# Kernel tuning notes

Measured on AMD Instinct MI355X. Metric: run time of the kernel, lower is better.

The kernel has to match this reference:

```python
import jax, jax.numpy as jnp
import numpy as np

EPS_NORM = 1e-12   # F.normalize default eps
EPS_ABS = 1e-08


def _l2_normalize(x, axis):
    n = jnp.sqrt(jnp.sum(x * x, axis=axis, keepdims=True))
    return x / jnp.maximum(n, EPS_NORM)


def setup_inputs() -> dict:
    key = jax.random.key(0)
    k1, k2 = jax.random.split(key)
    B, D, H, W = 32, 256, 32, 32
    S = 2048
    features = jax.random.normal(k1, (B, D, H, W), dtype=jnp.float32)
    memory = jax.random.truncated_normal(k2, -2.0, 2.0, (S, D), dtype=jnp.float32) * 0.02
    return {"features": features, "memory": memory}


def reference(features, memory):
    shrink_threshold = 0.0025
    shrink_gamma = 2.0
    temperature = 0.05
    B, D, H, W = features.shape
    S = memory.shape[0]

    # (B,D,H,W) -> (B*H*W, D)
    query = jnp.transpose(features, (0, 2, 3, 1)).reshape(B * H * W, D)

    # addressing: cosine similarity / temperature -> softmax over slots
    q = _l2_normalize(query, axis=1)
    m = _l2_normalize(memory, axis=1)
    sim = (q @ m.T) / temperature                      # [N, S]
    weights = jax.nn.softmax(sim, axis=1)

    # retrieval + soft shrinkage
    retrieved = weights @ memory                       # [N, D]
    a = jnp.abs(retrieved)
    lam = jnp.clip(shrink_gamma * shrink_threshold / (a + EPS_ABS), 0.0, 1.0)
    retrieved = jnp.sign(retrieved) * jax.nn.relu(a * (1.0 - lam))

    # entropy of addressing weights
    entropy = -jnp.mean(jnp.sum(weights * jnp.log(weights + EPS_ABS), axis=1))

    retrieved = jnp.transpose(retrieved.reshape(B, H, W, D), (0, 3, 1, 2))
    weights_image = weights.reshape(B, H * W, S).mean(axis=1)
    return retrieved, entropy, weights_image
```

## Files before the change

kernel.cpp:

```cpp
#include <hip/hip_runtime.h>
#include <cstdint>
#include <cstddef>

#define D_DIM 256
#define S_SLOTS 2048
#define HW_PIX 1024
#define OUT_ENT_IDX 8388608
#define OUT_WIMG_IDX 8388609

using short8 = __attribute__((ext_vector_type(8))) short;
using f32x4  = __attribute__((ext_vector_type(4))) float;

__device__ __forceinline__ unsigned short f2bf(float x) {
    union { float f; unsigned u; } v; v.f = x;
    unsigned r = v.u + 0x7FFF + ((v.u >> 16) & 1);
    return (unsigned short)(r >> 16);
}
__device__ __forceinline__ unsigned pack2(float lo, float hi) {
    return (unsigned)f2bf(lo) | ((unsigned)f2bf(hi) << 16);
}
__device__ __forceinline__ void gload16(const void* g, void* l) {
    __builtin_amdgcn_global_load_lds(
        (const __attribute__((address_space(1))) unsigned int*)g,
        (__attribute__((address_space(3))) unsigned int*)l, 16, 0, 0);
}

__global__ __launch_bounds__(64) void k_prep(const float* __restrict__ mem,
                                             unsigned short* __restrict__ mhatg,
                                             unsigned short* __restrict__ mblkg) {
    const int s = blockIdx.x;
    const int l = threadIdx.x;
    const float4 v = reinterpret_cast<const float4*>(mem + (size_t)s * D_DIM)[l];
    float ss = v.x*v.x + v.y*v.y + v.z*v.z + v.w*v.w;
#pragma unroll
    for (int o = 32; o > 0; o >>= 1) ss += __shfl_xor(ss, o);
    const float sc = 20.0f / fmaxf(sqrtf(ss), 1e-12f);
    {
        ushort4 o;
        o.x = f2bf(v.x*sc); o.y = f2bf(v.y*sc); o.z = f2bf(v.z*sc); o.w = f2bf(v.w*sc);
        const int chunk = (l >> 1) ^ (s & 7);
        char* dst = (char*)mhatg + (size_t)s * 512 + (chunk << 4) + 8 * (l & 1);
        *reinterpret_cast<ushort4*>(dst) = o;
    }
    {
        const int tile = s >> 6, sloc = s & 63;
        char* base = (char*)mblkg + (size_t)tile * 32768;
        const float vv[4] = {v.x, v.y, v.z, v.w};
#pragma unroll
        for (int i = 0; i < 4; ++i) {
            const int d = 4*l + i;
            const int byteoff = d * 128 + ((sloc * 2) ^ ((d & 7) << 4));
            *reinterpret_cast<unsigned short*>(base + byteoff) = f2bf(vv[i]);
        }
    }
}

__device__ __forceinline__ void qkt(const char* mh, const short8 (&qfrag)[2][8],
                                    int srow, int g, int l15, f32x4 (&acc)[2][2]) {
#pragma unroll
    for (int kk = 0; kk < 8; ++kk) {
        const int c0 = ((4*kk + g) ^ (l15 & 7)) << 4;
        const short8 a0 = *reinterpret_cast<const short8*>(mh + srow*512 + c0);
        const short8 a1 = *reinterpret_cast<const short8*>(mh + (srow+16)*512 + c0);
        acc[0][0] = __builtin_amdgcn_mfma_f32_16x16x32_bf16(a0, qfrag[0][kk], acc[0][0], 0,0,0);
        acc[0][1] = __builtin_amdgcn_mfma_f32_16x16x32_bf16(a0, qfrag[1][kk], acc[0][1], 0,0,0);
        acc[1][0] = __builtin_amdgcn_mfma_f32_16x16x32_bf16(a1, qfrag[0][kk], acc[1][0], 0,0,0);
        acc[1][1] = __builtin_amdgcn_mfma_f32_16x16x32_bf16(a1, qfrag[1][kk], acc[1][1], 0,0,0);
    }
}

__global__ __launch_bounds__(512, 2) void k_main(
    const float* __restrict__ feat, const char* __restrict__ mhat_g,
    const char* __restrict__ mblk_g, float* __restrict__ out)
{
    extern __shared__ char dyn[];
    __shared__ float sm_norm[512];
    __shared__ float qs_lds[128];
    __shared__ float zb[2][4][2][16];
    __shared__ float ub[2][4][2][16];
    __shared__ float rZbuf[128];
    __shared__ float entb[4];

    const int tid  = threadIdx.x;
    const int lane = tid & 63;
    const int w    = tid >> 6;
    const int wq   = w & 3;
    const int ws   = w >> 2;
    const int l15  = lane & 15;
    const int g    = (lane >> 4) & 3;
    const int blk  = blockIdx.x;
    const int b    = blk >> 3;
    const int p0   = (blk & 7) * 128;
    const float* fbase = feat + (size_t)b * (D_DIM * HW_PIX);
    float* wimg_g = out + OUT_WIMG_IDX;

    {
        const int dp = tid >> 7, pp = tid & 127;
        const float* fp = fbase + (size_t)(dp*64)*HW_PIX + p0 + pp;
        float ss = 0.f;
#pragma unroll 8
        for (int d = 0; d < 64; ++d) { const float v = fp[(size_t)d*HW_PIX]; ss += v*v; }
        sm_norm[dp*128 + pp] = ss;
    }
    __syncthreads();
    if (tid < 128) {
        const float n2 = sm_norm[tid] + sm_norm[128+tid] + sm_norm[256+tid] + sm_norm[384+tid];
        qs_lds[tid] = 1.0f / fmaxf(sqrtf(n2), 1e-12f);
    }
    __syncthreads();

    short8 qfrag[2][8];
#pragma unroll
    for (int tq = 0; tq < 2; ++tq) {
        const int q = 32*wq + 16*tq + l15;
        const float qs = qs_lds[q];
        const float* fq = fbase + p0 + q;
#pragma unroll
        for (int kk = 0; kk < 8; ++kk) {
            union { short8 s; unsigned u[4]; } fr;
#pragma unroll
            for (int jp = 0; jp < 4; ++jp) {
                const int d = 32*kk + 8*g + 2*jp;
                fr.u[jp] = pack2(fq[(size_t)d*HW_PIX] * qs, fq[(size_t)(d+1)*HW_PIX] * qs);
            }
            qfrag[tq][kk] = fr.s;
        }
    }

    const int srow = 32*ws + l15;

    float Zp[2] = {0.f, 0.f}, Up[2] = {0.f, 0.f};
    for (int st = 0; st < 32; ++st) {
        const char* gsrc = mhat_g + (size_t)st * 32768;
#pragma unroll
        for (int i = 0; i < 4; ++i)
            gload16(gsrc + tid*16 + i*8192, dyn + tid*16 + i*8192);
        __syncthreads();
        f32x4 acc[2][2] = {};
        qkt(dyn, qfrag, srow, g, l15, acc);
#pragma unroll
        for (int ts = 0; ts < 2; ++ts)
#pragma unroll
            for (int tq = 0; tq < 2; ++tq)
#pragma unroll
                for (int r = 0; r < 4; ++r) {
                    const float sim = acc[ts][tq][r];
                    const float e = __expf(sim);
                    Zp[tq] += e; Up[tq] += e * sim;
                }
        __syncthreads();
    }
#pragma unroll
    for (int tq = 0; tq < 2; ++tq) {
        Zp[tq] += __shfl_xor(Zp[tq], 16); Zp[tq] += __shfl_xor(Zp[tq], 32);
        Up[tq] += __shfl_xor(Up[tq], 16); Up[tq] += __shfl_xor(Up[tq], 32);
    }
    if (lane < 16) {
#pragma unroll
        for (int tq = 0; tq < 2; ++tq) {
            zb[ws][wq][tq][lane] = Zp[tq];
            ub[ws][wq][tq][lane] = Up[tq];
        }
    }
    __syncthreads();
    float rZ[2], rZw[2];
    {
        float Zf[2], Uf[2];
#pragma unroll
        for (int tq = 0; tq < 2; ++tq) {
            Zf[tq] = Zp[tq] + zb[1-ws][wq][tq][l15];
            Uf[tq] = Up[tq] + ub[1-ws][wq][tq][l15];
            rZ[tq] = 1.0f / Zf[tq];
            rZw[tq] = rZ[tq] * (1.0f/1024.0f);
        }
        if (ws == 0 && lane < 16) {
            rZbuf[32*wq + l15]      = rZ[0];
            rZbuf[32*wq + 16 + l15] = rZ[1];
            float ent = 0.f;
#pragma unroll
            for (int tq = 0; tq < 2; ++tq) ent += __logf(Zf[tq]) - Uf[tq] * rZ[tq];
            ent += __shfl_xor(ent, 1); ent += __shfl_xor(ent, 2);
            ent += __shfl_xor(ent, 4); ent += __shfl_xor(ent, 8);
            if (lane == 0) entb[wq] = ent;
        }
    }
    __syncthreads();
    if (tid == 0)
        atomicAdd(out + OUT_ENT_IDX, (entb[0]+entb[1]+entb[2]+entb[3]) * (1.0f/32768.0f));

    f32x4 acc_o[2][16] = {};
    for (int st = 0; st < 32; ++st) {
        const char* gsrcA = mhat_g + (size_t)st * 32768;
        const char* gsrcB = mblk_g + (size_t)st * 32768;
#pragma unroll
        for (int i = 0; i < 4; ++i) {
            gload16(gsrcA + tid*16 + i*8192, dyn + tid*16 + i*8192);
            gload16(gsrcB + tid*16 + i*8192, dyn + 33792 + tid*16 + i*8192);
        }
        __syncthreads();
        f32x4 acc[2][2] = {};
        qkt(dyn, qfrag, srow, g, l15, acc);
        float ev[2][2][4];
#pragma unroll
        for (int ts = 0; ts < 2; ++ts)
#pragma unroll
            for (int tq = 0; tq < 2; ++tq)
#pragma unroll
                for (int r = 0; r < 4; ++r)
                    ev[ts][tq][r] = __expf(acc[ts][tq][r]);
        __syncthreads();
#pragma unroll
        for (int ts = 0; ts < 2; ++ts)
#pragma unroll
            for (int tq = 0; tq < 2; ++tq) {
                const int q = 32*wq + 16*tq + l15;
#pragma unroll
                for (int r = 0; r < 4; ++r) {
                    const int s = 32*ws + 16*ts + 4*g + r;
                    *reinterpret_cast<float*>(dyn + s*528 + q*4) = ev[ts][tq][r] * rZw[tq];
                }
            }
        __syncthreads();
        {
            const int s_r = tid >> 3, qc = tid & 7;
            const char* pr = dyn + s_r*528 + qc*64;
            float ps = 0.f;
#pragma unroll
            for (int i = 0; i < 4; ++i) {
                const f32x4 v = *reinterpret_cast<const f32x4*>(pr + i*16);
                ps += v[0] + v[1] + v[2] + v[3];
            }
            ps += __shfl_xor(ps, 1); ps += __shfl_xor(ps, 2); ps += __shfl_xor(ps, 4);
            if (qc == 0) atomicAdd(wimg_g + (size_t)b*2048 + st*64 + s_r, ps);
        }
        short8 pfrag[2];
#pragma unroll
        for (int tq = 0; tq < 2; ++tq) {
            const unsigned u00 = pack2(ev[0][tq][0], ev[0][tq][1]);
            const unsigned u01 = pack2(ev[0][tq][2], ev[0][tq][3]);
            const unsigned u10 = pack2(ev[1][tq][0], ev[1][tq][1]);
            const unsigned u11 = pack2(ev[1][tq][2], ev[1][tq][3]);
            const int sA = l15 + 32*(g & 1);
            const int sB = sA + 16;
            const unsigned a00 = __shfl((int)u00, sA), a10 = __shfl((int)u10, sA);
            const unsigned a01 = __shfl((int)u01, sA), a11 = __shfl((int)u11, sA);
            const unsigned b00 = __shfl((int)u00, sB), b10 = __shfl((int)u10, sB);
            const unsigned b01 = __shfl((int)u01, sB), b11 = __shfl((int)u11, sB);
            const bool hi = (lane & 32) != 0;
            union { short8 s; unsigned u[4]; } fr;
            fr.u[0] = hi ? a10 : a00;
            fr.u[1] = hi ? a11 : a01;
            fr.u[2] = hi ? b10 : b00;
            fr.u[3] = hi ? b11 : b01;
            pfrag[tq] = fr.s;
        }
#pragma unroll
        for (int Dt = 0; Dt < 16; ++Dt) {
            const int d = 16*Dt + l15;
            const int byteoff = 33792 + d*128 + (((4*ws + g) ^ (l15 & 7)) << 4);
            const short8 bf = *reinterpret_cast<const short8*>(dyn + byteoff);
            acc_o[0][Dt] = __builtin_amdgcn_mfma_f32_16x16x32_bf16(pfrag[0], bf, acc_o[0][Dt], 0,0,0);
            acc_o[1][Dt] = __builtin_amdgcn_mfma_f32_16x16x32_bf16(pfrag[1], bf, acc_o[1][Dt], 0,0,0);
        }
        __syncthreads();
    }

    float rZq[2][4];
#pragma unroll
    for (int tq = 0; tq < 2; ++tq)
#pragma unroll
        for (int r = 0; r < 4; ++r)
            rZq[tq][r] = rZbuf[32*wq + 16*tq + 4*g + r];

#pragma unroll
    for (int Dt = 0; Dt < 16; ++Dt) {
        if (ws == 1) {
#pragma unroll
            for (int tq = 0; tq < 2; ++tq)
                *reinterpret_cast<f32x4*>(dyn + ((wq*2 + tq)*64 + lane)*16) = acc_o[tq][Dt];
        }
        __syncthreads();
        if (ws == 0) {
#pragma unroll
            for (int tq = 0; tq < 2; ++tq) {
                const f32x4 other = *reinterpret_cast<const f32x4*>(dyn + ((wq*2 + tq)*64 + lane)*16);
#pragma unroll
                for (int r = 0; r < 4; ++r) {
                    const float o = (acc_o[tq][Dt][r] + other[r]) * rZq[tq][r];
                    const float a = fabsf(o);
                    const float lam = fminf(0.005f / (a + 1e-8f), 1.0f);
                    const float val = copysignf(a * (1.0f - lam), o);
                    const int q = 32*wq + 16*tq + 4*g + r;
                    *reinterpret_cast<float*>(dyn + 8192 + q*84 + l15*4) = val;
                }
            }
        }
        __syncthreads();
#pragma unroll
        for (int i = 0; i < 4; ++i) {
            const int flat = i*512 + tid;
            const int dd = flat >> 7, q = flat & 127;
            const float val = *reinterpret_cast<const float*>(dyn + 8192 + q*84 + dd*4);
            out[((size_t)b*256 + Dt*16 + dd)*HW_PIX + p0 + q] = val;
        }
        __syncthreads();
    }
}

extern "C" void kernel_launch(void* const* d_in, const int* in_sizes, int n_in,
                              void* d_out, int out_size, void* d_ws, size_t ws_size,
                              hipStream_t stream) {
    const float* feat = (const float*)d_in[0];
    const float* mem  = (const float*)d_in[1];
    float* out = (float*)d_out;

    unsigned short* mhat_g = (unsigned short*)d_ws;
    unsigned short* mblk_g = (unsigned short*)((char*)d_ws + (1 << 20));

    hipMemsetAsync((char*)d_out + (size_t)OUT_ENT_IDX * 4, 0,
                   (size_t)(1 + 32 * S_SLOTS) * 4, stream);

    k_prep<<<S_SLOTS, 64, 0, stream>>>(mem, mhat_g, mblk_g);

    const int lds_bytes = 66560;
    hipFuncSetAttribute((const void*)k_main,
                        hipFuncAttributeMaxDynamicSharedMemorySize, lds_bytes);
    k_main<<<256, 512, lds_bytes, stream>>>(feat, (const char*)mhat_g,
                                            (const char*)mblk_g, out);
}
```

Before: 240.8 us.

## Double-buffer memory tiles in LDS, accumulate weights_image in LDS, coalesce prep

Both passes over the memory slots now use double-buffered LDS tiles, with the next tile's async global-to-LDS load issued before computing on the current one. This removes one barrier per iteration and hides load latency. The weights_image column sums now come from wave shuffles into a per-block LDS array, flushed once to global with atomics, replacing the LDS transpose, two extra barriers and per-tile global atomics. The prep kernel stages eight rows in LDS so it can write full 16-byte swizzled chunks with 256 blocks. The cost is a much larger dynamic LDS footprint, which limits residency to one block per CU.

After: 241.9 us. No clear change (+0.5%).

```diff
diff --git a/kernel.cpp b/kernel.cpp
--- a/kernel.cpp
+++ b/kernel.cpp
@@ -8,6 +8,11 @@
 #define OUT_ENT_IDX 8388608
 #define OUT_WIMG_IDX 8388609
 
+#define BUFA_OFF(b) ((b) * 32768)
+#define BUFB_OFF(b) (65536 + (b) * 32768)
+#define WIMG_OFF    131072
+#define DYN_BYTES   139264
+
 using short8 = __attribute__((ext_vector_type(8))) short;
 using f32x4  = __attribute__((ext_vector_type(4))) float;
 
@@ -28,30 +33,49 @@
 __global__ __launch_bounds__(64) void k_prep(const float* __restrict__ mem,
                                              unsigned short* __restrict__ mhatg,
                                              unsigned short* __restrict__ mblkg) {
-    const int s = blockIdx.x;
-    const int l = threadIdx.x;
-    const float4 v = reinterpret_cast<const float4*>(mem + (size_t)s * D_DIM)[l];
-    float ss = v.x*v.x + v.y*v.y + v.z*v.z + v.w*v.w;
-#pragma unroll
-    for (int o = 32; o > 0; o >>= 1) ss += __shfl_xor(ss, o);
-    const float sc = 20.0f / fmaxf(sqrtf(ss), 1e-12f);
+    __shared__ float lm[8 * 257];
+    __shared__ float scl[8];
+    const int l = threadIdx.x, blk = blockIdx.x;
+    const int tile = blk >> 3, oct = blk & 7;
+    const int s0 = tile * 64 + oct * 8;
+    const float* src = mem + (size_t)s0 * D_DIM;
+#pragma unroll
+    for (int i = 0; i < 8; ++i) {
+        const int f4 = i * 64 + l;
+        const int r = f4 >> 6, dq = (f4 & 63) * 4;
+        const float4 v = reinterpret_cast<const float4*>(src)[f4];
+        float* p = lm + r * 257 + dq;
+        p[0] = v.x; p[1] = v.y; p[2] = v.z; p[3] = v.w;
+    }
+    __syncthreads();
     {
-        ushort4 o;
-        o.x = f2bf(v.x*sc); o.y = f2bf(v.y*sc); o.z = f2bf(v.z*sc); o.w = f2bf(v.w*sc);
-        const int chunk = (l >> 1) ^ (s & 7);
-        char* dst = (char*)mhatg + (size_t)s * 512 + (chunk << 4) + 8 * (l & 1);
-        *reinterpret_cast<ushort4*>(dst) = o;
-    }
-    {
-        const int tile = s >> 6, sloc = s & 63;
-        char* base = (char*)mblkg + (size_t)tile * 32768;
-        const float vv[4] = {v.x, v.y, v.z, v.w};
-#pragma unroll
-        for (int i = 0; i < 4; ++i) {
-            const int d = 4*l + i;
-            const int byteoff = d * 128 + ((sloc * 2) ^ ((d & 7) << 4));
-            *reinterpret_cast<unsigned short*>(base + byteoff) = f2bf(vv[i]);
-        }
+        const int r = l >> 3, pp = l & 7;
+        float ss = 0.f;
+#pragma unroll 8
+        for (int d = 0; d < 32; ++d) { const float v = lm[r * 257 + pp * 32 + d]; ss += v * v; }
+        ss += __shfl_xor(ss, 1); ss += __shfl_xor(ss, 2); ss += __shfl_xor(ss, 4);
+        if (pp == 0) scl[r] = 20.0f / fmaxf(sqrtf(ss), 1e-12f);
+    }
+    __syncthreads();
+#pragma unroll
+    for (int i = 0; i < 4; ++i) {
+        const int c = i * 64 + l, r = c >> 5, k = c & 31;
+        const int s_g = s0 + r;
+        const float sc = scl[r];
+        const float* p = lm + r * 257 + ((k ^ (s_g & 7)) * 8);
+        union { short8 s; unsigned short h[8]; } o;
+#pragma unroll
+        for (int j = 0; j < 8; ++j) o.h[j] = f2bf(p[j] * sc);
+        *reinterpret_cast<short8*>((char*)mhatg + (size_t)s_g * 512 + k * 16) = o.s;
+    }
+#pragma unroll
+    for (int i = 0; i < 4; ++i) {
+        const int d = i * 64 + l;
+        const int k = oct ^ (d & 7);
+        union { short8 s; unsigned short h[8]; } o;
+#pragma unroll
+        for (int j = 0; j < 8; ++j) o.h[j] = f2bf(lm[j * 257 + d]);
+        *reinterpret_cast<short8*>((char*)mblkg + (size_t)tile * 32768 + d * 128 + k * 16) = o.s;
     }
 }
 
@@ -59,13 +83,13 @@
                                     int srow, int g, int l15, f32x4 (&acc)[2][2]) {
 #pragma unroll
     for (int kk = 0; kk < 8; ++kk) {
-        const int c0 = ((4*kk + g) ^ (l15 & 7)) << 4;
-        const short8 a0 = *reinterpret_cast<const short8*>(mh + srow*512 + c0);
-        const short8 a1 = *reinterpret_cast<const short8*>(mh + (srow+16)*512 + c0);
-        acc[0][0] = __builtin_amdgcn_mfma_f32_16x16x32_bf16(a0, qfrag[0][kk], acc[0][0], 0,0,0);
-        acc[0][1] = __builtin_amdgcn_mfma_f32_16x16x32_bf16(a0, qfrag[1][kk], acc[0][1], 0,0,0);
-        acc[1][0] = __builtin_amdgcn_mfma_f32_16x16x32_bf16(a1, qfrag[0][kk], acc[1][0], 0,0,0);
-        acc[1][1] = __builtin_amdgcn_mfma_f32_16x16x32_bf16(a1, qfrag[1][kk], acc[1][1], 0,0,0);
+        const int c0 = ((4 * kk + g) ^ (l15 & 7)) << 4;
+        const short8 a0 = *reinterpret_cast<const short8*>(mh + srow * 512 + c0);
+        const short8 a1 = *reinterpret_cast<const short8*>(mh + (srow + 16) * 512 + c0);
+        acc[0][0] = __builtin_amdgcn_mfma_f32_16x16x32_bf16(a0, qfrag[0][kk], acc[0][0], 0, 0, 0);
+        acc[0][1] = __builtin_amdgcn_mfma_f32_16x16x32_bf16(a0, qfrag[1][kk], acc[0][1], 0, 0, 0);
+        acc[1][0] = __builtin_amdgcn_mfma_f32_16x16x32_bf16(a1, qfrag[0][kk], acc[1][0], 0, 0, 0);
+        acc[1][1] = __builtin_amdgcn_mfma_f32_16x16x32_bf16(a1, qfrag[1][kk], acc[1][1], 0, 0, 0);
     }
 }
 
@@ -92,19 +116,39 @@
     const int b    = blk >> 3;
     const int p0   = (blk & 7) * 128;
     const float* fbase = feat + (size_t)b * (D_DIM * HW_PIX);
-    float* wimg_g = out + OUT_WIMG_IDX;
+    float* wimg_l = reinterpret_cast<float*>(dyn + WIMG_OFF);
+
+    auto stageA = [&](int st, int buf) {
+        const char* gsrc = mhat_g + (size_t)st * 32768;
+        char* ldst = dyn + BUFA_OFF(buf);
+#pragma unroll
+        for (int i = 0; i < 4; ++i)
+            gload16(gsrc + tid * 16 + i * 8192, ldst + tid * 16 + i * 8192);
+    };
+    auto stageB = [&](int st, int buf) {
+        const char* gsrc = mblk_g + (size_t)st * 32768;
+        char* ldst = dyn + BUFB_OFF(buf);
+#pragma unroll
+        for (int i = 0; i < 4; ++i)
+            gload16(gsrc + tid * 16 + i * 8192, ldst + tid * 16 + i * 8192);
+    };
+
+    stageA(0, 0);
+
+#pragma unroll
+    for (int i = 0; i < 4; ++i) wimg_l[i * 512 + tid] = 0.f;
 
     {
         const int dp = tid >> 7, pp = tid & 127;
-        const float* fp = fbase + (size_t)(dp*64)*HW_PIX + p0 + pp;
+        const float* fp = fbase + (size_t)(dp * 64) * HW_PIX + p0 + pp;
         float ss = 0.f;
 #pragma unroll 8
-        for (int d = 0; d < 64; ++d) { const float v = fp[(size_t)d*HW_PIX]; ss += v*v; }
-        sm_norm[dp*128 + pp] = ss;
+        for (int d = 0; d < 64; ++d) { const float v = fp[(size_t)d * HW_PIX]; ss += v * v; }
+        sm_norm[dp * 128 + pp] = ss;
     }
     __syncthreads();
     if (tid < 128) {
-        const float n2 = sm_norm[tid] + sm_norm[128+tid] + sm_norm[256+tid] + sm_norm[384+tid];
+        const float n2 = sm_norm[tid] + sm_norm[128 + tid] + sm_norm[256 + tid] + sm_norm[384 + tid];
         qs_lds[tid] = 1.0f / fmaxf(sqrtf(n2), 1e-12f);
     }
     __syncthreads();
@@ -112,7 +156,7 @@
     short8 qfrag[2][8];
 #pragma unroll
     for (int tq = 0; tq < 2; ++tq) {
-        const int q = 32*wq + 16*tq + l15;
+        const int q = 32 * wq + 16 * tq + l15;
         const float qs = qs_lds[q];
         const float* fq = fbase + p0 + q;
 #pragma unroll
@@ -120,24 +164,22 @@
             union { short8 s; unsigned u[4]; } fr;
 #pragma unroll
             for (int jp = 0; jp < 4; ++jp) {
-                const int d = 32*kk + 8*g + 2*jp;
-                fr.u[jp] = pack2(fq[(size_t)d*HW_PIX] * qs, fq[(size_t)(d+1)*HW_PIX] * qs);
+                const int d = 32 * kk + 8 * g + 2 * jp;
+                fr.u[jp] = pack2(fq[(size_t)d * HW_PIX] * qs, fq[(size_t)(d + 1) * HW_PIX] * qs);
             }
             qfrag[tq][kk] = fr.s;
         }
     }
 
-    const int srow = 32*ws + l15;
+    const int srow = 32 * ws + l15;
 
     float Zp[2] = {0.f, 0.f}, Up[2] = {0.f, 0.f};
+    __syncthreads();
+    int cur = 0;
     for (int st = 0; st < 32; ++st) {
-        const char* gsrc = mhat_g + (size_t)st * 32768;
-#pragma unroll
-        for (int i = 0; i < 4; ++i)
-            gload16(gsrc + tid*16 + i*8192, dyn + tid*16 + i*8192);
-        __syncthreads();
+        if (st < 31) stageA(st + 1, cur ^ 1);
         f32x4 acc[2][2] = {};
-        qkt(dyn, qfrag, srow, g, l15, acc);
+        qkt(dyn + BUFA_OFF(cur), qfrag, srow, g, l15, acc);
 #pragma unroll
         for (int ts = 0; ts < 2; ++ts)
 #pragma unroll
@@ -149,7 +191,11 @@
                     Zp[tq] += e; Up[tq] += e * sim;
                 }
         __syncthreads();
-    }
+        cur ^= 1;
+    }
+
+    stageA(0, 0); stageB(0, 0);
+
 #pragma unroll
     for (int tq = 0; tq < 2; ++tq) {
         Zp[tq] += __shfl_xor(Zp[tq], 16); Zp[tq] += __shfl_xor(Zp[tq], 32);
@@ -168,14 +214,14 @@
         float Zf[2], Uf[2];
 #pragma unroll
         for (int tq = 0; tq < 2; ++tq) {
-            Zf[tq] = Zp[tq] + zb[1-ws][wq][tq][l15];
-            Uf[tq] = Up[tq] + ub[1-ws][wq][tq][l15];
+            Zf[tq] = Zp[tq] + zb[1 - ws][wq][tq][l15];
+            Uf[tq] = Up[tq] + ub[1 - ws][wq][tq][l15];
             rZ[tq] = 1.0f / Zf[tq];
-            rZw[tq] = rZ[tq] * (1.0f/1024.0f);
+            rZw[tq] = rZ[tq] * (1.0f / 1024.0f);
         }
         if (ws == 0 && lane < 16) {
-            rZbuf[32*wq + l15]      = rZ[0];
-            rZbuf[32*wq + 16 + l15] = rZ[1];
+            rZbuf[32 * wq + l15]      = rZ[0];
+            rZbuf[32 * wq + 16 + l15] = rZ[1];
             float ent = 0.f;
 #pragma unroll
             for (int tq = 0; tq < 2; ++tq) ent += __logf(Zf[tq]) - Uf[tq] * rZ[tq];
@@ -186,20 +232,14 @@
     }
     __syncthreads();
     if (tid == 0)
-        atomicAdd(out + OUT_ENT_IDX, (entb[0]+entb[1]+entb[2]+entb[3]) * (1.0f/32768.0f));
+        atomicAdd(out + OUT_ENT_IDX, (entb[0] + entb[1] + entb[2] + entb[3]) * (1.0f / 32768.0f));
 
     f32x4 acc_o[2][16] = {};
+    cur = 0;
     for (int st = 0; st < 32; ++st) {
-        const char* gsrcA = mhat_g + (size_t)st * 32768;
-        const char* gsrcB = mblk_g + (size_t)st * 32768;
-#pragma unroll
-        for (int i = 0; i < 4; ++i) {
-            gload16(gsrcA + tid*16 + i*8192, dyn + tid*16 + i*8192);
-            gload16(gsrcB + tid*16 + i*8192, dyn + 33792 + tid*16 + i*8192);
-        }
-        __syncthreads();
+        if (st < 31) { stageA(st + 1, cur ^ 1); stageB(st + 1, cur ^ 1); }
         f32x4 acc[2][2] = {};
-        qkt(dyn, qfrag, srow, g, l15, acc);
+        qkt(dyn + BUFA_OFF(cur), qfrag, srow, g, l15, acc);
         float ev[2][2][4];
 #pragma unroll
         for (int ts = 0; ts < 2; ++ts)
@@ -208,31 +248,20 @@
 #pragma unroll
                 for (int r = 0; r < 4; ++r)
                     ev[ts][tq][r] = __expf(acc[ts][tq][r]);
-        __syncthreads();
+
 #pragma unroll
         for (int ts = 0; ts < 2; ++ts)
 #pragma unroll
-            for (int tq = 0; tq < 2; ++tq) {
-                const int q = 32*wq + 16*tq + l15;
-#pragma unroll
-                for (int r = 0; r < 4; ++r) {
-                    const int s = 32*ws + 16*ts + 4*g + r;
-                    *reinterpret_cast<float*>(dyn + s*528 + q*4) = ev[ts][tq][r] * rZw[tq];
-                }
+            for (int r = 0; r < 4; ++r) {
+                float wsum = ev[ts][0][r] * rZw[0] + ev[ts][1][r] * rZw[1];
+                wsum += __shfl_xor(wsum, 1);
+                wsum += __shfl_xor(wsum, 2);
+                wsum += __shfl_xor(wsum, 4);
+                wsum += __shfl_xor(wsum, 8);
+                if (l15 == 0)
+                    atomicAdd(&wimg_l[st * 64 + 32 * ws + 16 * ts + 4 * g + r], wsum);
             }
-        __syncthreads();
-        {
-            const int s_r = tid >> 3, qc = tid & 7;
-            const char* pr = dyn + s_r*528 + qc*64;
-            float ps = 0.f;
-#pragma unroll
-            for (int i = 0; i < 4; ++i) {
-                const f32x4 v = *reinterpret_cast<const f32x4*>(pr + i*16);
-                ps += v[0] + v[1] + v[2] + v[3];
-            }
-            ps += __shfl_xor(ps, 1); ps += __shfl_xor(ps, 2); ps += __shfl_xor(ps, 4);
-            if (qc == 0) atomicAdd(wimg_g + (size_t)b*2048 + st*64 + s_r, ps);
-        }
+
         short8 pfrag[2];
 #pragma unroll
         for (int tq = 0; tq < 2; ++tq) {
@@ -240,7 +269,7 @@
             const unsigned u01 = pack2(ev[0][tq][2], ev[0][tq][3]);
             const unsigned u10 = pack2(ev[1][tq][0], ev[1][tq][1]);
             const unsigned u11 = pack2(ev[1][tq][2], ev[1][tq][3]);
-            const int sA = l15 + 32*(g & 1);
+            const int sA = l15 + 32 * (g & 1);
             const int sB = sA + 16;
             const unsigned a00 = __shfl((int)u00, sA), a10 = __shfl((int)u10, sA);
             const unsigned a01 = __shfl((int)u01, sA), a11 = __shfl((int)u11, sA);
@@ -254,15 +283,26 @@
             fr.u[3] = hi ? b11 : b01;
             pfrag[tq] = fr.s;
         }
+        const char* mb = dyn + BUFB_OFF(cur);
+        const int cswz = (((4 * ws + g) ^ (l15 & 7)) << 4);
 #pragma unroll
         for (int Dt = 0; Dt < 16; ++Dt) {
-            const int d = 16*Dt + l15;
-            const int byteoff = 33792 + d*128 + (((4*ws + g) ^ (l15 & 7)) << 4);
-            const short8 bf = *reinterpret_cast<const short8*>(dyn + byteoff);
-            acc_o[0][Dt] = __builtin_amdgcn_mfma_f32_16x16x32_bf16(pfrag[0], bf, acc_o[0][Dt], 0,0,0);
-            acc_o[1][Dt] = __builtin_amdgcn_mfma_f32_16x16x32_bf16(pfrag[1], bf, acc_o[1][Dt], 0,0,0);
-        }
-        __syncthreads();
+            const int d = 16 * Dt + l15;
+            const short8 bf = *reinterpret_cast<const short8*>(mb + d * 128 + cswz);
+            acc_o[0][Dt] = __builtin_amdgcn_mfma_f32_16x16x32_bf16(pfrag[0], bf, acc_o[0][Dt], 0, 0, 0);
+            acc_o[1][Dt] = __builtin_amdgcn_mfma_f32_16x16x32_bf16(pfrag[1], bf, acc_o[1][Dt], 0, 0, 0);
+        }
+        __syncthreads();
+        cur ^= 1;
+    }
+
+    {
+        float* wimg_gb = out + OUT_WIMG_IDX + (size_t)b * S_SLOTS;
+#pragma unroll
+        for (int i = 0; i < 4; ++i) {
+            const int s = i * 512 + tid;
+            atomicAdd(wimg_gb + s, wimg_l[s]);
+        }
     }
 
     float rZq[2][4];
@@ -270,38 +310,38 @@
     for (int tq = 0; tq < 2; ++tq)
 #pragma unroll
         for (int r = 0; r < 4; ++r)
-            rZq[tq][r] = rZbuf[32*wq + 16*tq + 4*g + r];
+            rZq[tq][r] = rZbuf[32 * wq + 16 * tq + 4 * g + r];
 
 #pragma unroll
     for (int Dt = 0; Dt < 16; ++Dt) {
         if (ws == 1) {
 #pragma unroll
             for (int tq = 0; tq < 2; ++tq)
-                *reinterpret_cast<f32x4*>(dyn + ((wq*2 + tq)*64 + lane)*16) = acc_o[tq][Dt];
+                *reinterpret_cast<f32x4*>(dyn + ((wq * 2 + tq) * 64 + lane) * 16) = acc_o[tq][Dt];
         }
         __syncthreads();
         if (ws == 0) {
 #pragma unroll
             for (int tq = 0; tq < 2; ++tq) {
-                const f32x4 other = *reinterpret_cast<const f32x4*>(dyn + ((wq*2 + tq)*64 + lane)*16);
+                const f32x4 other = *reinterpret_cast<const f32x4*>(dyn + ((wq * 2 + tq) * 64 + lane) * 16);
 #pragma unroll
                 for (int r = 0; r < 4; ++r) {
                     const float o = (acc_o[tq][Dt][r] + other[r]) * rZq[tq][r];
                     const float a = fabsf(o);
                     const float lam = fminf(0.005f / (a + 1e-8f), 1.0f);
                     const float val = copysignf(a * (1.0f - lam), o);
-                    const int q = 32*wq + 16*tq + 4*g + r;
-                    *reinterpret_cast<float*>(dyn + 8192 + q*84 + l15*4) = val;
+                    const int q = 32 * wq + 16 * tq + 4 * g + r;
+                    *reinterpret_cast<float*>(dyn + 8192 + q * 84 + l15 * 4) = val;
                 }
             }
         }
         __syncthreads();
 #pragma unroll
         for (int i = 0; i < 4; ++i) {
-            const int flat = i*512 + tid;
+            const int flat = i * 512 + tid;
             const int dd = flat >> 7, q = flat & 127;
-            const float val = *reinterpret_cast<const float*>(dyn + 8192 + q*84 + dd*4);
-            out[((size_t)b*256 + Dt*16 + dd)*HW_PIX + p0 + q] = val;
+            const float val = *reinterpret_cast<const float*>(dyn + 8192 + q * 84 + dd * 4);
+            out[((size_t)b * 256 + Dt * 16 + dd) * HW_PIX + p0 + q] = val;
         }
         __syncthreads();
     }
@@ -320,11 +360,10 @@
     hipMemsetAsync((char*)d_out + (size_t)OUT_ENT_IDX * 4, 0,
                    (size_t)(1 + 32 * S_SLOTS) * 4, stream);
 
-    k_prep<<<S_SLOTS, 64, 0, stream>>>(mem, mhat_g, mblk_g);
-
-    const int lds_bytes = 66560;
+    k_prep<<<256, 64, 0, stream>>>(mem, mhat_g, mblk_g);
+
     hipFuncSetAttribute((const void*)k_main,
-                        hipFuncAttributeMaxDynamicSharedMemorySize, lds_bytes);
-    k_main<<<256, 512, lds_bytes, stream>>>(feat, (const char*)mhat_g,
+                        hipFuncAttributeMaxDynamicSharedMemorySize, DYN_BYTES);
+    k_main<<<256, 512, DYN_BYTES, stream>>>(feat, (const char*)mhat_g,
                                             (const char*)mblk_g, out);
 }
```
